# Performance work log

Hardware: AMD Instinct MI355X
Metric: run time of the kernel (lower is better)

The kernel has to match this reference:

```python
import math
import jax, jax.numpy as jnp
import numpy as np

B, S, M, D, H = 4, 1024, 8, 64, 8
NF = D // 2  # n_freq = head_dim // 2
BANDWIDTH = 1.0


def setup_inputs() -> dict:
    key = jax.random.key(0)
    ks = jax.random.split(key, 12)
    n = lambda k, shp, sc=1.0: (jax.random.normal(k, shp, dtype=jnp.float32) * sc)
    w_scale = 0.02  # typical init scale for linear weights
    return {
        'q_atoms': n(ks[0], (B, S, M, D)),
        'q_logw': n(ks[1], (B, S, M)),
        'k_atoms': n(ks[2], (B, S, M, D)),
        'k_logw': n(ks[3], (B, S, M)),
        'v_atoms': n(ks[4], (B, S, M, D)),
        'v_logw': n(ks[5], (B, S, M)),
        'Wq': n(ks[6], (H * D, D), w_scale),   # torch Linear weight [out, in]
        'Wk': n(ks[7], (H * D, D), w_scale),
        'Wv': n(ks[8], (H * D, D), w_scale),
        'Wo': n(ks[9], (D, H * D), w_scale),
        'Ww': n(ks[10], (M, D), w_scale * 0.1),  # w_proj.weight scaled by 0.1
        'freqs': n(ks[11], (H, D, NF), 1.0 / BANDWIDTH),  # buffer
    }


def reference(q_atoms, q_logw, k_atoms, k_logw, v_atoms, v_logw,
              Wq, Wk, Wv, Wo, Ww, freqs):
    rff_scale = 1.0 / math.sqrt(NF)
    attn_scale = 1.0 / math.sqrt(D)

    q_w = jax.nn.softmax(q_logw, axis=-1)  # [B,S,M]
    k_w = jax.nn.softmax(k_logw, axis=-1)

    def proj(x, W):  # x: [B,S,M,D], W: [H*D, D] -> [B,S,M,H,D]
        return jnp.einsum('bsmd,ed->bsme', x, W).reshape(B, -1, M, H, D)

    qa = proj(q_atoms, Wq)
    ka = proj(k_atoms, Wk)
    va = proj(v_atoms, Wv)  # [B,S,M,H,D]

    def rff_encode(atoms, weights):
        # atoms: [B,S,M,H,D], weights: [B,S,M] -> [B,H,S,F] with F=D
        p = jnp.einsum('bsmhd,hdf->bsmhf', atoms, freqs)
        phi = jnp.concatenate([jnp.cos(p), jnp.sin(p)], axis=-1) * rff_scale
        z = jnp.einsum('bsmhf,bsm->bshf', phi, weights)
        return z.transpose(0, 2, 1, 3)

    q_enc = rff_encode(qa, q_w)  # [B,H,S,D]
    k_enc = rff_encode(ka, k_w)

    attn = jax.nn.softmax(
        jnp.einsum('bhqf,bhkf->bhqk', q_enc, k_enc) * attn_scale, axis=-1)

    # attn @ values, keeping atom dim m: [B,S,M,H,D]
    out = jnp.einsum('bhqk,bkmhd->bqmhd', attn, va)
    out = out.reshape(B, S, M, H * D)
    out_atoms = out @ Wo.T                  # [B,S,M,D]
    out_features = out_atoms.mean(axis=2)   # [B,S,D]
    new_log_weights = q_logw + out_features @ Ww.T  # [B,S,M]
    return out_atoms, new_log_weights
```

## Files before the change

kernel.cpp:

```cpp
#include <hip/hip_runtime.h>
#include <hip/hip_bf16.h>

typedef __hip_bfloat16 bf16;
typedef __attribute__((ext_vector_type(8))) short short8;
typedef __attribute__((ext_vector_type(4))) float floatx4;

#define CB 4
#define CS 1024
#define CM 8
#define CD 64
#define CH 8
#define CNF 32
#define CHD 512

#define OB_STRIDE 520
#define OS_STRIDE 68
#define AT_STRIDE 72

__device__ __forceinline__ float b2f(bf16 x) { return __bfloat162float(x); }
__device__ __forceinline__ float us2f(unsigned short u) {
    union { unsigned int i; float f; } v; v.i = ((unsigned int)u) << 16; return v.f;
}
__device__ __forceinline__ floatx4 mfma16(short8 a, short8 b, floatx4 c) {
    return __builtin_amdgcn_mfma_f32_16x16x32_bf16(a, b, c, 0, 0, 0);
}


__global__ __launch_bounds__(256) void prep(const float* __restrict__ Wq,
                                            const float* __restrict__ Wk,
                                            const float* __restrict__ freqs,
                                            const float* __restrict__ Wo,
                                            const float* __restrict__ Wv,
                                            bf16* __restrict__ Fqb,
                                            bf16* __restrict__ Fkb,
                                            bf16* __restrict__ Cf) {
    int bx = blockIdx.x, t = threadIdx.x;
    if (bx < 128) {
        int which = bx >> 6, h = (bx >> 3) & 7, ec = bx & 7;
        const float* W = which ? Wk : Wq;
        bf16* Fb = which ? Fkb : Fqb;
        int f = t & 31, el = t >> 5;
        int e = ec * 8 + el;
        float acc = 0.f;
        for (int d = 0; d < 64; ++d)
            acc += W[(h * 64 + d) * 64 + e] * freqs[(h * 64 + d) * 32 + f];
        int ntile = h * 2 + (f >> 4);
        int half = e >> 5, quad = (e >> 3) & 3, j = e & 7;
        Fb[(ntile * 2 + half) * 512 + quad * 128 + (f & 15) * 8 + j] = __float2bfloat16(acc);
    } else {
        int fid = ((bx - 128) * 256 + t) * 8;
        int o = fid >> 9, rem = fid & 511, h = rem >> 6, e0 = rem & 63;
        const float* wo = Wo + o * 512 + h * 64;
        float accv[8];
        #pragma unroll
        for (int i = 0; i < 8; ++i) accv[i] = 0.f;
        for (int d = 0; d < 64; ++d) {
            float wod = wo[d];
            const float* wv = Wv + (size_t)(h * 64 + d) * 64 + e0;
            #pragma unroll
            for (int i = 0; i < 8; ++i) accv[i] += wod * wv[i];
        }
        int k = h * 64 + e0;
        int ot = o >> 4, r0 = o & 15, ks = k >> 5, qd = (k >> 3) & 3;
        union { bf16 ob[8]; short8 s8; } pk;
        #pragma unroll
        for (int i = 0; i < 8; ++i) pk.ob[i] = __float2bfloat16(accv[i]);
        *(short8*)(Cf + (ot * 16 + ks) * 512 + qd * 128 + r0 * 8) = pk.s8;
    }
}

__global__ __launch_bounds__(256) void encvp(const float* __restrict__ qa_in,
                                             const float* __restrict__ ql,
                                             const float* __restrict__ ka_in,
                                             const float* __restrict__ kl,
                                             const bf16* __restrict__ Fqb,
                                             const bf16* __restrict__ Fkb,
                                             bf16* __restrict__ qf,
                                             bf16* __restrict__ kf,
                                             const float* __restrict__ va_in,
                                             bf16* __restrict__ vaf) {
    __shared__ __align__(16) bf16 smem[20480];
    int t = threadIdx.x;
    int w = t >> 6, l = t & 63;
    int quad = l >> 4, r = l & 15;

    if (blockIdx.x < 1024) {
        int blk = blockIdx.x;
        int xbase = blk * 4;
        int b = xbase >> 10, s0 = xbase & 1023;
        float* wgtF = (float*)smem;
        bf16* atq = smem + 128;
        bf16* atk = smem + 128 + 2304;
        bf16* zL  = smem + 128 + 4608;
        int tw = w & 1, nb = (w >> 1) * 8;

        {
            const float* srcq = qa_in + (size_t)(blk * 32) * 64;
            const float* srck = ka_in + (size_t)(blk * 32) * 64;
            #pragma unroll
            for (int j = 0; j < 2; ++j) {
                int idx4 = j * 256 + t;
                int flat = idx4 * 4;
                int row = flat >> 6, e = flat & 63;
                float4 vq = ((const float4*)srcq)[idx4];
                float4 vk = ((const float4*)srck)[idx4];
                union { bf16 ob[4]; uint2 u; } pq, pk2;
                pq.ob[0] = __float2bfloat16(vq.x); pq.ob[1] = __float2bfloat16(vq.y);
                pq.ob[2] = __float2bfloat16(vq.z); pq.ob[3] = __float2bfloat16(vq.w);
                pk2.ob[0] = __float2bfloat16(vk.x); pk2.ob[1] = __float2bfloat16(vk.y);
                pk2.ob[2] = __float2bfloat16(vk.z); pk2.ob[3] = __float2bfloat16(vk.w);
                *(uint2*)(atq + row * AT_STRIDE + e) = pq.u;
                *(uint2*)(atk + row * AT_STRIDE + e) = pk2.u;
            }
        }
        if (t < 64) {
            int which = t >> 5, row = t & 31;
            int si = row >> 3, m = row & 7;
            const float* lwp = (which ? kl : ql) + (size_t)(xbase + si) * 8;
            float lw[8]; float mx = -1e30f;
            #pragma unroll
            for (int j = 0; j < 8; ++j) { lw[j] = lwp[j]; mx = fmaxf(mx, lw[j]); }
            float sm = 0.f;
            #pragma unroll
            for (int j = 0; j < 8; ++j) sm += __expf(lw[j] - mx);
            const float rs = 0.17677669529663687f;
            float osc = which ? rs : rs * 0.125f;
            wgtF[which * 32 + row] = __expf(lw[m] - mx) * (osc / sm);
        }
        __syncthreads();

        for (int which = 0; which < 2; ++which) {
            const bf16* atb2 = which ? atk : atq;
            const bf16* Fb = which ? Fkb : Fqb;

            short8 a0 = *(const short8*)(atb2 + (tw * 16 + r) * AT_STRIDE + quad * 8);
            short8 a1 = *(const short8*)(atb2 + (tw * 16 + r) * AT_STRIDE + quad * 8 + 32);

            floatx4 acc[8];
            #pragma unroll
            for (int nt = 0; nt < 8; ++nt) {
                int ntile = nb + nt;
                short8 b0 = *(const short8*)(Fb + (ntile * 2 + 0) * 512 + l * 8);
                short8 b1 = *(const short8*)(Fb + (ntile * 2 + 1) * 512 + l * 8);
                floatx4 c = {0.f, 0.f, 0.f, 0.f};
                c = mfma16(a0, b0, c);
                c = mfma16(a1, b1, c);
                acc[nt] = c;
            }

            float wv[4];
            #pragma unroll
            for (int reg = 0; reg < 4; ++reg)
                wv[reg] = wgtF[which * 32 + tw * 16 + quad * 4 + reg];

            int si = tw * 2 + (quad >> 1);
            int iss = quad & 1;
            #pragma unroll
            for (int nt = 0; nt < 8; ++nt) {
                int n = (nb + nt) * 16 + r;
                int h = n >> 5, f = n & 31;
                float zc = 0.f, zs = 0.f;
                #pragma unroll
                for (int reg = 0; reg < 4; ++reg) {
                    float sv, cv;
                    __sincosf(acc[nt][reg], &sv, &cv);
                    zc += wv[reg] * cv;
                    zs += wv[reg] * sv;
                }
                zc += __shfl_xor(zc, 16);
                zs += __shfl_xor(zs, 16);
                float val = iss ? zs : zc;
                zL[((which * 4 + si) * 8 + h) * 64 + f + 32 * iss] = __float2bfloat16(val);
            }
        }
        __syncthreads();

        #pragma unroll
        for (int rep = 0; rep < 2; ++rep) {
            int idx = rep * 256 + t;
            int row = idx >> 3, c = idx & 7;
            int which = row >> 5, si = (row >> 3) & 3, h = row & 7;
            bf16* enc = which ? kf : qf;
            short8 v = *(const short8*)(zL + row * 64 + c * 8);
            int s = s0 + si;
            int bh = b * 8 + h;
            int kt = s >> 4, half = c >> 2, qd = c & 3;
            *(short8*)(enc + ((size_t)((bh * 64 + kt) * 2 + half)) * 512
                           + (qd * 16 + (s & 15)) * 8) = v;
        }
    } else {
        int vp = blockIdx.x - 1024;
        int b = vp >> 5, sc = vp & 31;
        const float* src = va_in + ((size_t)(b * 1024 + sc * 32)) * 512;
        #pragma unroll
        for (int rep = 0; rep < 2; ++rep) {
            int nn = rep * 256 + t;
            int m = nn >> 6, e = nn & 63, nblk = nn >> 4, rr = nn & 15;
            bf16* dchunk = vaf + ((size_t)((b * 32 + nblk) * 32 + sc)) * 512;
            #pragma unroll
            for (int qd = 0; qd < 4; ++qd) {
                union { bf16 ob[8]; short8 s8; } pk;
                #pragma unroll
                for (int j = 0; j < 8; ++j) {
                    int s = qd * 8 + j;
                    pk.ob[j] = __float2bfloat16(src[(size_t)(s * 8 + m) * 64 + e]);
                }
                *(short8*)(dchunk + (qd * 16 + rr) * 8) = pk.s8;
            }
        }
    }
}

__global__ __launch_bounds__(512, 4) void attn_kern(const bf16* __restrict__ qf,
                                                    const bf16* __restrict__ kf,
                                                    const bf16* __restrict__ vaf,
                                                    bf16* __restrict__ tmpf) {
    int n = blockIdx.x;
    int bh = (n & 7) + 8 * (n >> 8);
    int qb = (n >> 3) & 31;
    int b = bh >> 3, h = bh & 7;

    __shared__ __align__(16) bf16 Sc[32 * 1024];
    __shared__ float sumW[8 * 32];
    __shared__ float invL[32];
    int t = threadIdx.x;
    int w = t >> 6, l = t & 63;
    int quad = l >> 4, r = l & 15;
    int k7 = r & 7;

    const bf16* qfb = qf + (size_t)(bh * 128 + qb * 4) * 512 + l * 8;
    short8 q0 = *(const short8*)(qfb);
    short8 q1 = *(const short8*)(qfb + 512);
    short8 q2 = *(const short8*)(qfb + 1024);
    short8 q3 = *(const short8*)(qfb + 1536);

    const bf16* kfb = kf + (size_t)(bh * 128) * 512 + l * 8;
    short8 kr[4][2];
    #pragma unroll
    for (int d = 0; d < 4; ++d) {
        kr[d][0] = *(const short8*)(kfb + (size_t)(w * 8 + d) * 1024);
        kr[d][1] = *(const short8*)(kfb + (size_t)(w * 8 + d) * 1024 + 512);
    }

    float ps0 = 0.f, ps1 = 0.f;
    #pragma unroll
    for (int i = 0; i < 8; ++i) {
        short8 k0 = kr[i & 3][0], k1 = kr[i & 3][1];
        if (i + 4 < 8) {
            kr[i & 3][0] = *(const short8*)(kfb + (size_t)(w * 8 + i + 4) * 1024);
            kr[i & 3][1] = *(const short8*)(kfb + (size_t)(w * 8 + i + 4) * 1024 + 512);
        }
        floatx4 c0 = {0.f, 0.f, 0.f, 0.f}, c1 = {0.f, 0.f, 0.f, 0.f};
        c0 = mfma16(k0, q0, c0); c0 = mfma16(k1, q1, c0);
        c1 = mfma16(k0, q2, c1); c1 = mfma16(k1, q3, c1);
        int ktl = w * 8 + i;
        int chunk = ktl * 2 + (quad >> 1);
        int sw = ((chunk ^ k7) << 3) + (quad & 1) * 4;
        union { uint2 u; bf16 bb[4]; } p0, p1;
        #pragma unroll
        for (int reg = 0; reg < 4; ++reg) {
            float e0 = __expf(c0[reg]);
            float e1 = __expf(c1[reg]);
            ps0 += e0; ps1 += e1;
            p0.bb[reg] = __float2bfloat16(e0);
            p1.bb[reg] = __float2bfloat16(e1);
        }
        *(uint2*)(Sc + r * 1024 + sw) = p0.u;
        *(uint2*)(Sc + (r + 16) * 1024 + sw) = p1.u;
    }
    ps0 += __shfl_xor(ps0, 16); ps0 += __shfl_xor(ps0, 32);
    ps1 += __shfl_xor(ps1, 16); ps1 += __shfl_xor(ps1, 32);
    if (l < 16) {
        sumW[w * 32 + r] = ps0;
        sumW[w * 32 + 16 + r] = ps1;
    }
    __syncthreads();

    if (t < 32) {
        float s = 0.f;
        #pragma unroll
        for (int w2 = 0; w2 < 8; ++w2) s += sumW[w2 * 32 + t];
        invL[t] = 1.f / s;
    }

    floatx4 acc0[4], acc1[4];
    #pragma unroll
    for (int nt = 0; nt < 4; ++nt) {
        acc0[nt] = (floatx4){0.f, 0.f, 0.f, 0.f};
        acc1[nt] = (floatx4){0.f, 0.f, 0.f, 0.f};
    }
    const bf16* vbase = vaf + ((size_t)(b * 32 + w * 4) * 32) * 512 + l * 8;
    short8 vr[4][4];
    #pragma unroll
    for (int d = 0; d < 4; ++d)
        #pragma unroll
        for (int nt = 0; nt < 4; ++nt)
            vr[d][nt] = *(const short8*)(vbase + nt * 16384 + d * 512);

    #pragma unroll
    for (int ks = 0; ks < 32; ++ks) {
        int pc = (((ks * 4 + quad) ^ k7) << 3);
        short8 pa0 = *(const short8*)(Sc + r * 1024 + pc);
        short8 pa1 = *(const short8*)(Sc + (16 + r) * 1024 + pc);
        __builtin_amdgcn_s_setprio(1);
        #pragma unroll
        for (int nt = 0; nt < 4; ++nt) {
            acc0[nt] = mfma16(pa0, vr[ks & 3][nt], acc0[nt]);
            acc1[nt] = mfma16(pa1, vr[ks & 3][nt], acc1[nt]);
        }
        __builtin_amdgcn_s_setprio(0);
        if (ks + 4 < 32) {
            #pragma unroll
            for (int nt = 0; nt < 4; ++nt)
                vr[ks & 3][nt] = *(const short8*)(vbase + nt * 16384 + (ks + 4) * 512);
        }
    }
    __syncthreads();

    float inv0[4], inv1[4];
    #pragma unroll
    for (int reg = 0; reg < 4; ++reg) {
        inv0[reg] = invL[quad * 4 + reg];
        inv1[reg] = invL[16 + quad * 4 + reg];
    }

    bf16* Ob = Sc;
    #pragma unroll
    for (int nt = 0; nt < 4; ++nt)
        #pragma unroll
        for (int reg = 0; reg < 4; ++reg) {
            int col = w * 64 + nt * 16 + r;
            int m = col >> 6, d = col & 63;
            int colS = m * 64 + ((d + m * 8) & 63);
            Ob[(quad * 4 + reg) * OB_STRIDE + colS] =
                __float2bfloat16(acc0[nt][reg] * inv0[reg]);
            Ob[(quad * 4 + reg + 16) * OB_STRIDE + colS] =
                __float2bfloat16(acc1[nt][reg] * inv1[reg]);
        }
    __syncthreads();

    #pragma unroll
    for (int i = 0; i < 4; ++i) {
        int ci = i * 8 + w;
        int lv = t & 63;
        int T = ci >> 1, khalf = ci & 1;
        int quadv = lv >> 4, rv = lv & 15;
        int p = rv >> 3, m = rv & 7;
        int q_local = T * 2 + p;
        int d0 = khalf * 32 + quadv * 8;
        int colS = m * 64 + ((d0 + m * 8) & 63);
        short8 v = *(const short8*)(Ob + q_local * OB_STRIDE + colS);
        int GT = b * 512 + qb * 16 + T;
        *(short8*)(tmpf + ((size_t)(GT * 16 + h * 2 + khalf)) * 512 + lv * 8) = v;
    }
}

__global__ __launch_bounds__(256) void finalize(const bf16* __restrict__ tmpf,
                                                const bf16* __restrict__ Cf,
                                                const float* __restrict__ Ww,
                                                const float* __restrict__ ql,
                                                float* __restrict__ out) {
    __shared__ __align__(16) float Os[64][OS_STRIDE];
    __shared__ float fs[8][64];
    int t = threadIdx.x;
    int w = t >> 6, l = t & 63;
    int quad = l >> 4, r = l & 15;
    size_t rowbase = (size_t)blockIdx.x * 64;

    floatx4 acc[4];
    #pragma unroll
    for (int nt = 0; nt < 4; ++nt) acc[nt] = (floatx4){0.f, 0.f, 0.f, 0.f};

    const bf16* afrag = tmpf + ((size_t)(blockIdx.x * 4 + w) * 16) * 512 + l * 8;
    const bf16* bfrag = Cf + l * 8;

    for (int ks = 0; ks < 16; ++ks) {
        short8 a = *(const short8*)(afrag + ks * 512);
        #pragma unroll
        for (int nt = 0; nt < 4; ++nt) {
            short8 bb = *(const short8*)(bfrag + (size_t)(nt * 16 + ks) * 512);
            acc[nt] = mfma16(a, bb, acc[nt]);
        }
    }
    #pragma unroll
    for (int nt = 0; nt < 4; ++nt)
        #pragma unroll
        for (int reg = 0; reg < 4; ++reg)
            Os[w * 16 + quad * 4 + reg][nt * 16 + r] = acc[nt][reg];
    __syncthreads();

    #pragma unroll
    for (int i = 0; i < 4; ++i) {
        int ch = i * 256 + t;
        int rr = ch >> 4, c4 = (ch & 15) * 4;
        float4 v = *(const float4*)&Os[rr][c4];
        *(float4*)(out + (rowbase + rr) * 64 + c4) = v;
    }

    {
        int g = t >> 5, oo = (t & 31) * 2;
        float f0 = 0.f, f1 = 0.f;
        #pragma unroll
        for (int m = 0; m < 8; ++m) {
            f0 += Os[g * 8 + m][oo];
            f1 += Os[g * 8 + m][oo + 1];
        }
        fs[g][oo] = f0 * 0.125f;
        fs[g][oo + 1] = f1 * 0.125f;
    }
    __syncthreads();

    if (t < 64) {
        int g = t >> 3, mm = t & 7;
        size_t x = (size_t)blockIdx.x * 8 + g;
        float nl = ql[x * 8 + mm];
        #pragma unroll
        for (int o = 0; o < 64; ++o) nl += fs[g][o] * Ww[mm * 64 + o];
        out[(size_t)CB * CS * CM * CD + x * 8 + mm] = nl;
    }
}

extern "C" void kernel_launch(void* const* d_in, const int* in_sizes, int n_in,
                              void* d_out, int out_size, void* d_ws, size_t ws_size,
                              hipStream_t stream) {
    const float* q_atoms = (const float*)d_in[0];
    const float* q_logw  = (const float*)d_in[1];
    const float* k_atoms = (const float*)d_in[2];
    const float* k_logw  = (const float*)d_in[3];
    const float* v_atoms = (const float*)d_in[4];
    const float* Wq = (const float*)d_in[6];
    const float* Wk = (const float*)d_in[7];
    const float* Wv = (const float*)d_in[8];
    const float* Wo = (const float*)d_in[9];
    const float* Ww = (const float*)d_in[10];
    const float* freqs = (const float*)d_in[11];

    bf16* Fqb = (bf16*)d_ws;
    bf16* Fkb = Fqb + 16384;
    bf16* qf = Fkb + 16384;
    bf16* kf = qf + 2097152;
    bf16* vaf = kf + 2097152;
    bf16* tmpf = vaf + 2097152 * 8;
    bf16* Cf = tmpf + 16777216;
    float* out = (float*)d_out;

    prep<<<144, 256, 0, stream>>>(Wq, Wk, freqs, Wo, Wv, Fqb, Fkb, Cf);
    encvp<<<1152, 256, 0, stream>>>(q_atoms, q_logw, k_atoms, k_logw,
                                    Fqb, Fkb, qf, kf,
                                    v_atoms, vaf);
    attn_kern<<<1024, 512, 0, stream>>>(qf, kf, vaf, tmpf);
    finalize<<<CB * CS / 8, 256, 0, stream>>>(tmpf, Cf, Ww, q_logw, out);
}
```

Before: 167.5 us.

## Double query tile per attention block and split key loop into halves

```diff
diff --git a/kernel.cpp b/kernel.cpp
--- a/kernel.cpp
+++ b/kernel.cpp
@@ -216,142 +216,150 @@
                                                     const bf16* __restrict__ vaf,
                                                     bf16* __restrict__ tmpf) {
     int n = blockIdx.x;
-    int bh = (n & 7) + 8 * (n >> 8);
-    int qb = (n >> 3) & 31;
-    int b = bh >> 3, h = bh & 7;
-
-    __shared__ __align__(16) bf16 Sc[32 * 1024];
-    __shared__ float sumW[8 * 32];
-    __shared__ float invL[32];
+    int xcd = n & 7, j = n >> 3;
+    int b = xcd & 3, p = xcd >> 2;
+    int h = j >> 3;
+    int qb = p * 8 + (j & 7);
+    int bh = b * 8 + h;
+
+    __shared__ __align__(16) bf16 Sc[64 * OB_STRIDE];
+    __shared__ float sumW[8 * 64];
+    __shared__ float invL[64];
     int t = threadIdx.x;
     int w = t >> 6, l = t & 63;
     int quad = l >> 4, r = l & 15;
     int k7 = r & 7;
 
-    const bf16* qfb = qf + (size_t)(bh * 128 + qb * 4) * 512 + l * 8;
-    short8 q0 = *(const short8*)(qfb);
-    short8 q1 = *(const short8*)(qfb + 512);
-    short8 q2 = *(const short8*)(qfb + 1024);
-    short8 q3 = *(const short8*)(qfb + 1536);
-
+    const bf16* qfb = qf + (size_t)(bh * 128 + qb * 8) * 512 + l * 8;
     const bf16* kfb = kf + (size_t)(bh * 128) * 512 + l * 8;
-    short8 kr[4][2];
-    #pragma unroll
-    for (int d = 0; d < 4; ++d) {
-        kr[d][0] = *(const short8*)(kfb + (size_t)(w * 8 + d) * 1024);
-        kr[d][1] = *(const short8*)(kfb + (size_t)(w * 8 + d) * 1024 + 512);
-    }
-
-    float ps0 = 0.f, ps1 = 0.f;
+    const bf16* vbase = vaf + ((size_t)(b * 32 + w * 4) * 32) * 512 + l * 8;
+
+    floatx4 acc[4][4];
+    #pragma unroll
+    for (int qt = 0; qt < 4; ++qt)
+        #pragma unroll
+        for (int nt = 0; nt < 4; ++nt) acc[qt][nt] = (floatx4){0.f, 0.f, 0.f, 0.f};
+    float ps[4] = {0.f, 0.f, 0.f, 0.f};
+
+    for (int khalf = 0; khalf < 2; ++khalf) {
+        {
+            short8 q[8];
+            #pragma unroll
+            for (int i = 0; i < 8; ++i) q[i] = *(const short8*)(qfb + i * 512);
+            short8 kr[4][2];
+            #pragma unroll
+            for (int d = 0; d < 4; ++d) {
+                kr[d][0] = *(const short8*)(kfb + (size_t)(khalf * 32 + w * 4 + d) * 1024);
+                kr[d][1] = *(const short8*)(kfb + (size_t)(khalf * 32 + w * 4 + d) * 1024 + 512);
+            }
+            #pragma unroll
+            for (int i = 0; i < 4; ++i) {
+                int ktl = w * 4 + i;
+                #pragma unroll
+                for (int qt = 0; qt < 4; ++qt) {
+                    floatx4 c = {0.f, 0.f, 0.f, 0.f};
+                    c = mfma16(kr[i][0], q[2 * qt], c);
+                    c = mfma16(kr[i][1], q[2 * qt + 1], c);
+                    int g = ktl * 2 + (quad >> 1);
+                    int sw = ((g ^ k7) << 3) + (quad & 1) * 4;
+                    union { uint2 u; bf16 bb[4]; } pp;
+                    #pragma unroll
+                    for (int reg = 0; reg < 4; ++reg) {
+                        float e = __expf(c[reg]);
+                        ps[qt] += e;
+                        pp.bb[reg] = __float2bfloat16(e);
+                    }
+                    *(uint2*)(Sc + (qt * 16 + r) * OB_STRIDE + sw) = pp.u;
+                }
+            }
+        }
+        if (khalf == 1) {
+            #pragma unroll
+            for (int qt = 0; qt < 4; ++qt) {
+                ps[qt] += __shfl_xor(ps[qt], 16);
+                ps[qt] += __shfl_xor(ps[qt], 32);
+            }
+            if (l < 16) {
+                #pragma unroll
+                for (int qt = 0; qt < 4; ++qt) sumW[w * 64 + qt * 16 + r] = ps[qt];
+            }
+        }
+        __syncthreads();
+        if (khalf == 1 && t < 64) {
+            float s = 0.f;
+            #pragma unroll
+            for (int w2 = 0; w2 < 8; ++w2) s += sumW[w2 * 64 + t];
+            invL[t] = 1.f / s;
+        }
+
+        {
+            short8 vr[2][4];
+            #pragma unroll
+            for (int d = 0; d < 2; ++d)
+                #pragma unroll
+                for (int nt = 0; nt < 4; ++nt)
+                    vr[d][nt] = *(const short8*)(vbase + nt * 16384
+                                                 + (khalf * 16 + d) * 512);
+            #pragma unroll
+            for (int ks = 0; ks < 16; ++ks) {
+                short8 pa[4];
+                #pragma unroll
+                for (int qt = 0; qt < 4; ++qt)
+                    pa[qt] = *(const short8*)(Sc + (qt * 16 + r) * OB_STRIDE
+                                              + (((ks * 4 + quad) ^ k7) << 3));
+                __builtin_amdgcn_s_setprio(1);
+                #pragma unroll
+                for (int nt = 0; nt < 4; ++nt)
+                    #pragma unroll
+                    for (int qt = 0; qt < 4; ++qt)
+                        acc[qt][nt] = mfma16(pa[qt], vr[ks & 1][nt], acc[qt][nt]);
+                __builtin_amdgcn_s_setprio(0);
+                if (ks + 2 < 16) {
+                    #pragma unroll
+                    for (int nt = 0; nt < 4; ++nt)
+                        vr[ks & 1][nt] = *(const short8*)(vbase + nt * 16384
+                                                          + (khalf * 16 + ks + 2) * 512);
+                }
+            }
+        }
+        __syncthreads();
+    }
+
+    float inv[4][4];
+    #pragma unroll
+    for (int qt = 0; qt < 4; ++qt)
+        #pragma unroll
+        for (int reg = 0; reg < 4; ++reg)
+            inv[qt][reg] = invL[qt * 16 + quad * 4 + reg];
+
+    bf16* Ob = Sc;
+    #pragma unroll
+    for (int qt = 0; qt < 4; ++qt)
+        #pragma unroll
+        for (int nt = 0; nt < 4; ++nt)
+            #pragma unroll
+            for (int reg = 0; reg < 4; ++reg) {
+                int col = w * 64 + nt * 16 + r;
+                int m = col >> 6, d = col & 63;
+                int colS = m * 64 + ((d + m * 8) & 63);
+                Ob[(qt * 16 + quad * 4 + reg) * OB_STRIDE + colS] =
+                    __float2bfloat16(acc[qt][nt][reg] * inv[qt][reg]);
+            }
+    __syncthreads();
+
     #pragma unroll
     for (int i = 0; i < 8; ++i) {
-        short8 k0 = kr[i & 3][0], k1 = kr[i & 3][1];
-        if (i + 4 < 8) {
-            kr[i & 3][0] = *(const short8*)(kfb + (size_t)(w * 8 + i + 4) * 1024);
-            kr[i & 3][1] = *(const short8*)(kfb + (size_t)(w * 8 + i + 4) * 1024 + 512);
-        }
-        floatx4 c0 = {0.f, 0.f, 0.f, 0.f}, c1 = {0.f, 0.f, 0.f, 0.f};
-        c0 = mfma16(k0, q0, c0); c0 = mfma16(k1, q1, c0);
-        c1 = mfma16(k0, q2, c1); c1 = mfma16(k1, q3, c1);
-        int ktl = w * 8 + i;
-        int chunk = ktl * 2 + (quad >> 1);
-        int sw = ((chunk ^ k7) << 3) + (quad & 1) * 4;
-        union { uint2 u; bf16 bb[4]; } p0, p1;
-        #pragma unroll
-        for (int reg = 0; reg < 4; ++reg) {
-            float e0 = __expf(c0[reg]);
-            float e1 = __expf(c1[reg]);
-            ps0 += e0; ps1 += e1;
-            p0.bb[reg] = __float2bfloat16(e0);
-            p1.bb[reg] = __float2bfloat16(e1);
-        }
-        *(uint2*)(Sc + r * 1024 + sw) = p0.u;
-        *(uint2*)(Sc + (r + 16) * 1024 + sw) = p1.u;
-    }
-    ps0 += __shfl_xor(ps0, 16); ps0 += __shfl_xor(ps0, 32);
-    ps1 += __shfl_xor(ps1, 16); ps1 += __shfl_xor(ps1, 32);
-    if (l < 16) {
-        sumW[w * 32 + r] = ps0;
-        sumW[w * 32 + 16 + r] = ps1;
-    }
-    __syncthreads();
-
-    if (t < 32) {
-        float s = 0.f;
-        #pragma unroll
-        for (int w2 = 0; w2 < 8; ++w2) s += sumW[w2 * 32 + t];
-        invL[t] = 1.f / s;
-    }
-
-    floatx4 acc0[4], acc1[4];
-    #pragma unroll
-    for (int nt = 0; nt < 4; ++nt) {
-        acc0[nt] = (floatx4){0.f, 0.f, 0.f, 0.f};
-        acc1[nt] = (floatx4){0.f, 0.f, 0.f, 0.f};
-    }
-    const bf16* vbase = vaf + ((size_t)(b * 32 + w * 4) * 32) * 512 + l * 8;
-    short8 vr[4][4];
-    #pragma unroll
-    for (int d = 0; d < 4; ++d)
-        #pragma unroll
-        for (int nt = 0; nt < 4; ++nt)
-            vr[d][nt] = *(const short8*)(vbase + nt * 16384 + d * 512);
-
-    #pragma unroll
-    for (int ks = 0; ks < 32; ++ks) {
-        int pc = (((ks * 4 + quad) ^ k7) << 3);
-        short8 pa0 = *(const short8*)(Sc + r * 1024 + pc);
-        short8 pa1 = *(const short8*)(Sc + (16 + r) * 1024 + pc);
-        __builtin_amdgcn_s_setprio(1);
-        #pragma unroll
-        for (int nt = 0; nt < 4; ++nt) {
-            acc0[nt] = mfma16(pa0, vr[ks & 3][nt], acc0[nt]);
-            acc1[nt] = mfma16(pa1, vr[ks & 3][nt], acc1[nt]);
-        }
-        __builtin_amdgcn_s_setprio(0);
-        if (ks + 4 < 32) {
-            #pragma unroll
-            for (int nt = 0; nt < 4; ++nt)
-                vr[ks & 3][nt] = *(const short8*)(vbase + nt * 16384 + (ks + 4) * 512);
-        }
-    }
-    __syncthreads();
-
-    float inv0[4], inv1[4];
-    #pragma unroll
-    for (int reg = 0; reg < 4; ++reg) {
-        inv0[reg] = invL[quad * 4 + reg];
-        inv1[reg] = invL[16 + quad * 4 + reg];
-    }
-
-    bf16* Ob = Sc;
-    #pragma unroll
-    for (int nt = 0; nt < 4; ++nt)
-        #pragma unroll
-        for (int reg = 0; reg < 4; ++reg) {
-            int col = w * 64 + nt * 16 + r;
-            int m = col >> 6, d = col & 63;
-            int colS = m * 64 + ((d + m * 8) & 63);
-            Ob[(quad * 4 + reg) * OB_STRIDE + colS] =
-                __float2bfloat16(acc0[nt][reg] * inv0[reg]);
-            Ob[(quad * 4 + reg + 16) * OB_STRIDE + colS] =
-                __float2bfloat16(acc1[nt][reg] * inv1[reg]);
-        }
-    __syncthreads();
-
-    #pragma unroll
-    for (int i = 0; i < 4; ++i) {
         int ci = i * 8 + w;
         int lv = t & 63;
-        int T = ci >> 1, khalf = ci & 1;
+        int T = ci >> 1, kh = ci & 1;
         int quadv = lv >> 4, rv = lv & 15;
-        int p = rv >> 3, m = rv & 7;
-        int q_local = T * 2 + p;
-        int d0 = khalf * 32 + quadv * 8;
+        int pp = rv >> 3, m = rv & 7;
+        int q_local = T * 2 + pp;
+        int d0 = kh * 32 + quadv * 8;
         int colS = m * 64 + ((d0 + m * 8) & 63);
         short8 v = *(const short8*)(Ob + q_local * OB_STRIDE + colS);
-        int GT = b * 512 + qb * 16 + T;
-        *(short8*)(tmpf + ((size_t)(GT * 16 + h * 2 + khalf)) * 512 + lv * 8) = v;
+        int GT = b * 512 + qb * 32 + T;
+        *(short8*)(tmpf + ((size_t)(GT * 16 + h * 2 + kh)) * 512 + lv * 8) = v;
     }
 }
 
@@ -448,6 +456,6 @@
     encvp<<<1152, 256, 0, stream>>>(q_atoms, q_logw, k_atoms, k_logw,
                                     Fqb, Fkb, qf, kf,
                                     v_atoms, vaf);
-    attn_kern<<<1024, 512, 0, stream>>>(qf, kf, vaf, tmpf);
+    attn_kern<<<512, 512, 0, stream>>>(qf, kf, vaf, tmpf);
     finalize<<<CB * CS / 8, 256, 0, stream>>>(tmpf, Cf, Ww, q_logw, out);
 }
```

Result: slower. 196.4 us (+17.3%).
